# Performance work log

Measured on AMD Instinct MI355X. Metric: run time of the kernel, lower is better.

## Reference

```python
import jax, jax.numpy as jnp
import numpy as np

EPS = 1e-6
B, N_NEG, H, D = 256, 1000, 3, 128
NUM_CLUSTER = (25000, 2500, 250)
NUM_IMG = 100000

def _l2norm(x):
    # matches torch F.normalize(dim=-1): x / max(||x||, 1e-12)
    n = jnp.sqrt(jnp.sum(x * x, axis=-1, keepdims=True))
    return x / jnp.maximum(n, 1e-12)

def setup_inputs() -> dict:
    key = jax.random.key(0)
    ks = jax.random.split(key, 10)
    return {
        "semantic_embs": jax.random.normal(ks[0], (B, H * D), dtype=jnp.float32),
        "centroids0": jax.random.normal(ks[1], (NUM_CLUSTER[0], D), dtype=jnp.float32),
        "centroids1": jax.random.normal(ks[2], (NUM_CLUSTER[1], D), dtype=jnp.float32),
        "centroids2": jax.random.normal(ks[3], (NUM_CLUSTER[2], D), dtype=jnp.float32),
        "im2cluster0": jax.random.randint(ks[4], (NUM_IMG,), 0, NUM_CLUSTER[0], dtype=jnp.int32),
        "im2cluster1": jax.random.randint(ks[5], (NUM_IMG,), 0, NUM_CLUSTER[1], dtype=jnp.int32),
        "im2cluster2": jax.random.randint(ks[6], (NUM_IMG,), 0, NUM_CLUSTER[2], dtype=jnp.int32),
        "index": jax.random.randint(ks[7], (B,), 0, NUM_IMG, dtype=jnp.int32),
        "neg_im2cluster": jax.random.randint(ks[8], (B, N_NEG, H), 0, min(NUM_CLUSTER), dtype=jnp.int32),
    }

def reference(semantic_embs, centroids0, centroids1, centroids2,
              im2cluster0, im2cluster1, im2cluster2, index, neg_im2cluster):
    cents = [centroids0, centroids1, centroids2]
    i2c = [im2cluster0, im2cluster1, im2cluster2]
    b = semantic_embs.shape[0]
    se = _l2norm(semantic_embs.reshape(b, H, D))                 # [B,H,D]

    # positive path: gather centroid of each sample's cluster per hierarchy
    pos = jnp.stack([_l2norm(cents[h][i2c[h][index]]) for h in range(H)], axis=1)  # [B,H,D]
    pos_path_sim = jnp.prod((jnp.sum(se * pos, axis=-1) + 1.0) * 0.5, axis=1)      # [B]
    pos_loss = -jnp.log(pos_path_sim + EPS)                                        # [B]

    # negative paths: gather sampled centroids per hierarchy
    neg = jnp.stack([_l2norm(cents[h][neg_im2cluster[:, :, h]]) for h in range(H)], axis=2)  # [B,N,H,D]
    neg_proto_sim = jnp.sum(se[:, None, :, :] * neg, axis=-1)                      # [B,N,H]
    neg_path_sim = jnp.prod((neg_proto_sim + 1.0) * 0.5, axis=-1)                  # [B,N]
    neg_loss = -jnp.log(1.0 - neg_path_sim + EPS)                                  # [B,N]

    # true_negative mask: neg path differs from positive path in any hierarchy
    pos_lab = jnp.stack([i2c[h][index] for h in range(H)], axis=-1)                # [B,H]
    tn = jnp.any(neg_im2cluster != pos_lab[:, None, :], axis=-1).astype(se.dtype)  # [B,N]
    neg_loss = jnp.sum(neg_loss * tn, axis=-1) / (jnp.sum(tn, axis=-1) + EPS)      # [B]

    return jnp.mean(jnp.stack([pos_loss, neg_loss], axis=-1))
```

## Files before the change

kernel.cpp:

```cpp
#include <hip/hip_runtime.h>
#include <math.h>

#define EPS   1e-6f
#define BB    256
#define NNEG  1000
#define HH    3
#define DD    128
#define NCN   250

__global__ void kA_prep(const float* __restrict__ c0,
                        const float* __restrict__ c1,
                        const float* __restrict__ c2,
                        float* __restrict__ centT,
                        float* __restrict__ out) {
    if (blockIdx.x == 0 && threadIdx.x == 0) out[0] = 0.0f;
    int wid  = blockIdx.x * 4 + (threadIdx.x >> 6);
    int lane = threadIdx.x & 63;
    if (wid >= HH * NCN) return;
    int h = (wid >= 2 * NCN) ? 2 : (wid >= NCN ? 1 : 0);
    int c = wid - h * NCN;
    const float* cp = (h == 0) ? c0 : (h == 1) ? c1 : c2;
    const float2 v = *(const float2*)(cp + (size_t)c * DD + lane * 2);
    float ss = v.x * v.x + v.y * v.y;
    #pragma unroll
    for (int off = 32; off; off >>= 1) ss += __shfl_xor(ss, off);
    float inv = 1.0f / fmaxf(sqrtf(ss), 1e-12f);
    float* base = centT + h * (DD * NCN);
    base[(lane * 2)     * NCN + c] = v.x * inv;
    base[(lane * 2 + 1) * NCN + c] = v.y * inv;
}

__global__ __launch_bounds__(512) void kB_main(
        const float* __restrict__ se,
        const float* __restrict__ c0,
        const float* __restrict__ c1,
        const float* __restrict__ c2,
        const int* __restrict__ i2c0,
        const int* __restrict__ i2c1,
        const int* __restrict__ i2c2,
        const int* __restrict__ index,
        const int* __restrict__ negc,
        const float* __restrict__ centT,
        float* __restrict__ out) {
    int b = blockIdx.x;
    int tid = threadIdx.x, wave = tid >> 6, lane = tid & 63;

    __shared__ float sse[HH * DD];
    __shared__ float ssim[HH * NCN];
    __shared__ int   snegc[NNEG * HH];
    __shared__ int   slab[HH];
    __shared__ float ph[HH];
    __shared__ float wL[8], wT[8];

    {
        const int4* src = (const int4*)(negc + (size_t)b * (NNEG * HH));
        int4* dst = (int4*)snegc;
        #pragma unroll
        for (int i = tid; i < (NNEG * HH) / 4; i += 512) dst[i] = src[i];
    }

    if (wave < HH) {
        int h = wave;
        const float2 s = *(const float2*)(se + (size_t)b * (HH * DD) + h * DD + lane * 2);
        float ssq = s.x * s.x + s.y * s.y;
        #pragma unroll
        for (int off = 32; off; off >>= 1) ssq += __shfl_xor(ssq, off);
        float inv = 1.0f / fmaxf(sqrtf(ssq), 1e-12f);
        float2 sn = make_float2(s.x * inv, s.y * inv);
        sse[h * DD + lane * 2]     = sn.x;
        sse[h * DD + lane * 2 + 1] = sn.y;

        int idx = index[b];
        const int*   ip = (h == 0) ? i2c0 : (h == 1) ? i2c1 : i2c2;
        const float* cp = (h == 0) ? c0   : (h == 1) ? c1   : c2;
        int cidx = ip[idx];
        const float2 cv = *(const float2*)(cp + (size_t)cidx * DD + lane * 2);
        float dot = sn.x * cv.x + sn.y * cv.y;
        float csq = cv.x * cv.x + cv.y * cv.y;
        #pragma unroll
        for (int off = 32; off; off >>= 1) {
            dot += __shfl_xor(dot, off);
            csq += __shfl_xor(csq, off);
        }
        if (lane == 0) {
            float invc = 1.0f / fmaxf(sqrtf(csq), 1e-12f);
            ph[h]   = (dot * invc + 1.0f) * 0.5f;
            slab[h] = cidx;
        }
    }
    __syncthreads();

    if (tid < HH * (NCN / 2)) {
        int h = tid / (NCN / 2);
        int p = tid - h * (NCN / 2);
        const float2* ct  = (const float2*)(centT + h * (DD * NCN)) + p;
        const float4* sh4 = (const float4*)(sse + h * DD);
        float dA = 0.0f, dB = 0.0f;
        #pragma unroll 4
        for (int dq = 0; dq < DD / 4; ++dq) {
            float4 s4 = sh4[dq];
            float2 v0 = ct[0 * (NCN / 2)];
            float2 v1 = ct[1 * (NCN / 2)];
            float2 v2 = ct[2 * (NCN / 2)];
            float2 v3 = ct[3 * (NCN / 2)];
            ct += 4 * (NCN / 2);
            dA = fmaf(s4.x, v0.x, dA); dB = fmaf(s4.x, v0.y, dB);
            dA = fmaf(s4.y, v1.x, dA); dB = fmaf(s4.y, v1.y, dB);
            dA = fmaf(s4.z, v2.x, dA); dB = fmaf(s4.z, v2.y, dB);
            dA = fmaf(s4.w, v3.x, dA); dB = fmaf(s4.w, v3.y, dB);
        }
        ssim[h * NCN + 2 * p]     = (dA + 1.0f) * 0.5f;
        ssim[h * NCN + 2 * p + 1] = (dB + 1.0f) * 0.5f;
    }
    __syncthreads();

    int l0 = slab[0], l1 = slab[1], l2 = slab[2];
    float accL = 0.0f, accT = 0.0f;
    #pragma unroll
    for (int k = 0; k < NNEG / 512 + 1; ++k) {
        int n = tid + k * 512;
        if (n < NNEG) {
            int i0 = snegc[n * 3], i1 = snegc[n * 3 + 1], i2 = snegc[n * 3 + 2];
            float p = ssim[i0] * ssim[NCN + i1] * ssim[2 * NCN + i2];
            if (i0 != l0 || i1 != l1 || i2 != l2) {
                accL -= logf(1.0f - p + EPS);
                accT += 1.0f;
            }
        }
    }
    #pragma unroll
    for (int off = 32; off; off >>= 1) {
        accL += __shfl_xor(accL, off);
        accT += __shfl_xor(accT, off);
    }
    if (lane == 0) { wL[wave] = accL; wT[wave] = accT; }
    __syncthreads();

    if (tid == 0) {
        float L = 0.0f, T = 0.0f;
        #pragma unroll
        for (int w = 0; w < 8; ++w) { L += wL[w]; T += wT[w]; }
        float neg_b = L / (T + EPS);
        float pos_b = -logf(ph[0] * ph[1] * ph[2] + EPS);
        atomicAdd(out, (pos_b + neg_b) * (1.0f / (2.0f * BB)));
    }
}

extern "C" void kernel_launch(void* const* d_in, const int* in_sizes, int n_in,
                              void* d_out, int out_size, void* d_ws, size_t ws_size,
                              hipStream_t stream) {
    const float* se    = (const float*)d_in[0];
    const float* c0    = (const float*)d_in[1];
    const float* c1    = (const float*)d_in[2];
    const float* c2    = (const float*)d_in[3];
    const int*   i2c0  = (const int*)d_in[4];
    const int*   i2c1  = (const int*)d_in[5];
    const int*   i2c2  = (const int*)d_in[6];
    const int*   index = (const int*)d_in[7];
    const int*   negc  = (const int*)d_in[8];

    float* centT = (float*)d_ws;
    float* out   = (float*)d_out;

    hipLaunchKernelGGL(kA_prep, dim3((HH * NCN + 3) / 4), dim3(256), 0, stream,
                       c0, c1, c2, centT, out);
    hipLaunchKernelGGL(kB_main, dim3(BB), dim3(512), 0, stream,
                       se, c0, c1, c2, i2c0, i2c1, i2c2, index, negc, centT, out);
}
```

Measured before the change: 91.47 us.

## Fuse centroid normalization into main kernel and replace atomic with reduce kernel

Removes the separate prep kernel that normalized and transposed the first 250 rows of each centroid table. The main kernel now reads the raw centroid rows directly, with 16 lanes cooperating per row to compute the dot product and the norm together. The final atomicAdd is replaced by per-sample partial sums and a small single-block reduce kernel. Each block now recomputes the centroid norms redundantly, but the workspace round trip and the atomic contention are gone.

```diff
diff --git a/kernel.cpp b/kernel.cpp
--- a/kernel.cpp
+++ b/kernel.cpp
@@ -8,29 +8,7 @@
 #define DD    128
 #define NCN   250
 
-__global__ void kA_prep(const float* __restrict__ c0,
-                        const float* __restrict__ c1,
-                        const float* __restrict__ c2,
-                        float* __restrict__ centT,
-                        float* __restrict__ out) {
-    if (blockIdx.x == 0 && threadIdx.x == 0) out[0] = 0.0f;
-    int wid  = blockIdx.x * 4 + (threadIdx.x >> 6);
-    int lane = threadIdx.x & 63;
-    if (wid >= HH * NCN) return;
-    int h = (wid >= 2 * NCN) ? 2 : (wid >= NCN ? 1 : 0);
-    int c = wid - h * NCN;
-    const float* cp = (h == 0) ? c0 : (h == 1) ? c1 : c2;
-    const float2 v = *(const float2*)(cp + (size_t)c * DD + lane * 2);
-    float ss = v.x * v.x + v.y * v.y;
-    #pragma unroll
-    for (int off = 32; off; off >>= 1) ss += __shfl_xor(ss, off);
-    float inv = 1.0f / fmaxf(sqrtf(ss), 1e-12f);
-    float* base = centT + h * (DD * NCN);
-    base[(lane * 2)     * NCN + c] = v.x * inv;
-    base[(lane * 2 + 1) * NCN + c] = v.y * inv;
-}
-
-__global__ __launch_bounds__(512) void kB_main(
+__global__ __launch_bounds__(512) void kMain(
         const float* __restrict__ se,
         const float* __restrict__ c0,
         const float* __restrict__ c1,
@@ -40,8 +18,7 @@
         const int* __restrict__ i2c2,
         const int* __restrict__ index,
         const int* __restrict__ negc,
-        const float* __restrict__ centT,
-        float* __restrict__ out) {
+        float* __restrict__ partial) {
     int b = blockIdx.x;
     int tid = threadIdx.x, wave = tid >> 6, lane = tid & 63;
 
@@ -90,27 +67,64 @@
     }
     __syncthreads();
 
-    if (tid < HH * (NCN / 2)) {
-        int h = tid / (NCN / 2);
-        int p = tid - h * (NCN / 2);
-        const float2* ct  = (const float2*)(centT + h * (DD * NCN)) + p;
-        const float4* sh4 = (const float4*)(sse + h * DD);
-        float dA = 0.0f, dB = 0.0f;
+    {
+        int g = tid >> 4, l = tid & 15;
+        float4 sa[HH], sb[HH];
+        #pragma unroll
+        for (int h = 0; h < HH; ++h) {
+            const float4* p4 = (const float4*)(sse + h * DD);
+            sa[h] = p4[l * 2];
+            sb[h] = p4[l * 2 + 1];
+        }
         #pragma unroll 4
-        for (int dq = 0; dq < DD / 4; ++dq) {
-            float4 s4 = sh4[dq];
-            float2 v0 = ct[0 * (NCN / 2)];
-            float2 v1 = ct[1 * (NCN / 2)];
-            float2 v2 = ct[2 * (NCN / 2)];
-            float2 v3 = ct[3 * (NCN / 2)];
-            ct += 4 * (NCN / 2);
-            dA = fmaf(s4.x, v0.x, dA); dB = fmaf(s4.x, v0.y, dB);
-            dA = fmaf(s4.y, v1.x, dA); dB = fmaf(s4.y, v1.y, dB);
-            dA = fmaf(s4.z, v2.x, dA); dB = fmaf(s4.z, v2.y, dB);
-            dA = fmaf(s4.w, v3.x, dA); dB = fmaf(s4.w, v3.y, dB);
+        for (int it = 0; it < 23; ++it) {
+            int cl = g + 32 * it;
+            int h = (cl >= 2 * NCN) ? 2 : (cl >= NCN ? 1 : 0);
+            int c = cl - h * NCN;
+            const float* cp = (h == 0) ? c0 : (h == 1) ? c1 : c2;
+            const float4* row = (const float4*)(cp + (size_t)c * DD);
+            float4 v0 = row[l * 2];
+            float4 v1 = row[l * 2 + 1];
+            float4 s0 = sa[h], s1 = sb[h];
+            float dot = v0.x * s0.x;
+            dot = fmaf(v0.y, s0.y, dot); dot = fmaf(v0.z, s0.z, dot); dot = fmaf(v0.w, s0.w, dot);
+            dot = fmaf(v1.x, s1.x, dot); dot = fmaf(v1.y, s1.y, dot);
+            dot = fmaf(v1.z, s1.z, dot); dot = fmaf(v1.w, s1.w, dot);
+            float nrm = v0.x * v0.x;
+            nrm = fmaf(v0.y, v0.y, nrm); nrm = fmaf(v0.z, v0.z, nrm); nrm = fmaf(v0.w, v0.w, nrm);
+            nrm = fmaf(v1.x, v1.x, nrm); nrm = fmaf(v1.y, v1.y, nrm);
+            nrm = fmaf(v1.z, v1.z, nrm); nrm = fmaf(v1.w, v1.w, nrm);
+            #pragma unroll
+            for (int off = 8; off; off >>= 1) {
+                dot += __shfl_xor(dot, off);
+                nrm += __shfl_xor(nrm, off);
+            }
+            if (l == 0)
+                ssim[cl] = (dot / fmaxf(sqrtf(nrm), 1e-12f) + 1.0f) * 0.5f;
         }
-        ssim[h * NCN + 2 * p]     = (dA + 1.0f) * 0.5f;
-        ssim[h * NCN + 2 * p + 1] = (dB + 1.0f) * 0.5f;
+        if (g < 14) {
+            int cl = g + 736;
+            int c = cl - 2 * NCN;
+            const float4* row = (const float4*)(c2 + (size_t)c * DD);
+            float4 v0 = row[l * 2];
+            float4 v1 = row[l * 2 + 1];
+            float4 s0 = sa[2], s1 = sb[2];
+            float dot = v0.x * s0.x;
+            dot = fmaf(v0.y, s0.y, dot); dot = fmaf(v0.z, s0.z, dot); dot = fmaf(v0.w, s0.w, dot);
+            dot = fmaf(v1.x, s1.x, dot); dot = fmaf(v1.y, s1.y, dot);
+            dot = fmaf(v1.z, s1.z, dot); dot = fmaf(v1.w, s1.w, dot);
+            float nrm = v0.x * v0.x;
+            nrm = fmaf(v0.y, v0.y, nrm); nrm = fmaf(v0.z, v0.z, nrm); nrm = fmaf(v0.w, v0.w, nrm);
+            nrm = fmaf(v1.x, v1.x, nrm); nrm = fmaf(v1.y, v1.y, nrm);
+            nrm = fmaf(v1.z, v1.z, nrm); nrm = fmaf(v1.w, v1.w, nrm);
+            #pragma unroll
+            for (int off = 8; off; off >>= 1) {
+                dot += __shfl_xor(dot, off);
+                nrm += __shfl_xor(nrm, off);
+            }
+            if (l == 0)
+                ssim[cl] = (dot / fmaxf(sqrtf(nrm), 1e-12f) + 1.0f) * 0.5f;
+        }
     }
     __syncthreads();
 
@@ -142,8 +156,20 @@
         for (int w = 0; w < 8; ++w) { L += wL[w]; T += wT[w]; }
         float neg_b = L / (T + EPS);
         float pos_b = -logf(ph[0] * ph[1] * ph[2] + EPS);
-        atomicAdd(out, (pos_b + neg_b) * (1.0f / (2.0f * BB)));
+        partial[b] = pos_b + neg_b;
     }
+}
+
+__global__ void kReduce(const float* __restrict__ partial, float* __restrict__ out) {
+    int tid = threadIdx.x, wave = tid >> 6, lane = tid & 63;
+    __shared__ float ws[4];
+    float v = partial[tid];
+    #pragma unroll
+    for (int off = 32; off; off >>= 1) v += __shfl_xor(v, off);
+    if (lane == 0) ws[wave] = v;
+    __syncthreads();
+    if (tid == 0)
+        out[0] = (ws[0] + ws[1] + ws[2] + ws[3]) * (1.0f / (2.0f * BB));
 }
 
 extern "C" void kernel_launch(void* const* d_in, const int* in_sizes, int n_in,
@@ -159,11 +185,11 @@
     const int*   index = (const int*)d_in[7];
     const int*   negc  = (const int*)d_in[8];
 
-    float* centT = (float*)d_ws;
-    float* out   = (float*)d_out;
+    float* partial = (float*)d_ws;
+    float* out     = (float*)d_out;
 
-    hipLaunchKernelGGL(kA_prep, dim3((HH * NCN + 3) / 4), dim3(256), 0, stream,
-                       c0, c1, c2, centT, out);
-    hipLaunchKernelGGL(kB_main, dim3(BB), dim3(512), 0, stream,
-                       se, c0, c1, c2, i2c0, i2c1, i2c2, index, negc, centT, out);
+    hipLaunchKernelGGL(kMain, dim3(BB), dim3(512), 0, stream,
+                       se, c0, c1, c2, i2c0, i2c1, i2c2, index, negc, partial);
+    hipLaunchKernelGGL(kReduce, dim3(1), dim3(256), 0, stream,
+                       partial, out);
 }
```

Result: slower. 95.14 us (+4.0%).
